# Kernel tuning notes

Hardware: AMD Instinct MI355X
Metric: run time of the kernel (lower is better)

The kernel has to match this reference:

```python
import jax, jax.numpy as jnp
import numpy as np

B, C, H, W, D = 8, 192, 128, 128, 64


def setup_inputs() -> dict:
    key = jax.random.key(0)
    ks = jax.random.split(key, 9)
    s = 0.1
    return {
        'x': jax.random.normal(ks[0], (B, C, H, W), jnp.float32),
        'Wi': jax.random.normal(ks[1], (D, C), jnp.float32) * s,   # proj_in weight
        'bi': jax.random.normal(ks[2], (D,), jnp.float32) * s,
        'W_ih': jax.random.normal(ks[3], (3 * D, D), jnp.float32) * s,  # GRUCell weight_ih (r,z,n)
        'W_hh': jax.random.normal(ks[4], (3 * D, D), jnp.float32) * s,  # GRUCell weight_hh
        'b_ih': jax.random.normal(ks[5], (3 * D,), jnp.float32) * s,
        'b_hh': jax.random.normal(ks[6], (3 * D,), jnp.float32) * s,
        'Wo': jax.random.normal(ks[7], (C, D), jnp.float32) * s,   # proj_out weight
        'bo': jax.random.normal(ks[8], (C,), jnp.float32) * s,
    }


def _gru_scan(seq, W_ih, W_hh, b_ih, b_hh):
    # seq: (N, T, D). PyTorch GRUCell gate order: r, z, n.
    N, T, Dh = seq.shape[0], seq.shape[1], W_hh.shape[1]
    x_gates = jnp.einsum('ntd,gd->ntg', seq, W_ih) + b_ih  # (N, T, 3D), precomputed
    h0 = jnp.zeros((N, Dh), seq.dtype)

    def step(h, xg):
        hg = h @ W_hh.T + b_hh
        xr, xz, xn = jnp.split(xg, 3, axis=-1)
        hr, hz, hn = jnp.split(hg, 3, axis=-1)
        r = jax.nn.sigmoid(xr + hr)
        z = jax.nn.sigmoid(xz + hz)
        n = jnp.tanh(xn + r * hn)
        h_new = (1.0 - z) * n + z * h
        return h_new, h_new

    _, hs = jax.lax.scan(step, h0, jnp.swapaxes(x_gates, 0, 1))  # (T, N, D)
    return jnp.swapaxes(hs, 0, 1)  # (N, T, D)


def _scan_direction(x, Wi, bi, W_ih, W_hh, b_ih, b_hh, Wo, bo, transpose, reverse):
    b, c, h, w = x.shape
    # arrange to (B, A, T, C): scan along T (W for row scans, H for column scans)
    xs = jnp.transpose(x, (0, 3, 2, 1)) if transpose else jnp.transpose(x, (0, 2, 3, 1))
    if reverse:
        xs = xs[:, :, ::-1, :]
    A, T = xs.shape[1], xs.shape[2]
    seq = xs.reshape(b * A, T, c) @ Wi.T + bi              # proj_in -> (N, T, D)
    hs = _gru_scan(seq, W_ih, W_hh, b_ih, b_hh)            # (N, T, D)
    out = hs @ Wo.T + bo                                   # proj_out -> (N, T, C)
    out = out.reshape(b, A, T, c)
    if reverse:
        out = out[:, :, ::-1, :]
    return jnp.transpose(out, (0, 3, 2, 1)) if transpose else jnp.transpose(out, (0, 3, 1, 2))


def reference(x, Wi, bi, W_ih, W_hh, b_ih, b_hh, Wo, bo):
    p = (Wi, bi, W_ih, W_hh, b_ih, b_hh, Wo, bo)
    right = _scan_direction(x, *p, transpose=False, reverse=False)
    down = _scan_direction(x, *p, transpose=True, reverse=False)
    left = _scan_direction(x, *p, transpose=False, reverse=True)
    up = _scan_direction(x, *p, transpose=True, reverse=True)
    return (right + down + left + up) / 4.0
```

## Files before the change

### kernel.cpp

```cpp
#include <hip/hip_runtime.h>

#define Cn   192
#define Dn   64
#define G3   192
#define HWn  16384
#define NSp  131072L
#define Tn   128

typedef unsigned short u16;
typedef __attribute__((ext_vector_type(8))) short s8v;
typedef __attribute__((ext_vector_type(4))) float f4v;

__device__ __forceinline__ float bf2f(u16 u){
  union { unsigned int i; float f; } v; v.i = ((unsigned int)u) << 16; return v.f;
}
__device__ __forceinline__ u16 f2bf(float f){
  union { float f; unsigned int u; } v; v.f = f;
  return (u16)((v.u + 0x7FFFu + ((v.u >> 16) & 1u)) >> 16);
}
__device__ __forceinline__ s8v load8_f32_as_bf16(const float* __restrict__ p){
  s8v r;
  #pragma unroll
  for (int i = 0; i < 8; i++) r[i] = (short)f2bf(p[i]);
  return r;
}
__device__ __forceinline__ float ex2f(float x){
#if __has_builtin(__builtin_amdgcn_exp2f)
  return __builtin_amdgcn_exp2f(x);
#else
  float r; asm("v_exp_f32 %0, %1" : "=v"(r) : "v"(x)); return r;
#endif
}
__device__ __forceinline__ float rcpa(float x){
#if __has_builtin(__builtin_amdgcn_rcpf)
  return __builtin_amdgcn_rcpf(x);
#else
  float r; asm("v_rcp_f32 %0, %1" : "=v"(r) : "v"(x)); return r;
#endif
}
__device__ __forceinline__ unsigned int pk2bf(float a, float b){
  unsigned int r; asm("v_cvt_pk_bf16_f32 %0, %1, %2" : "=v"(r) : "v"(a), "v"(b)); return r;
}

#define SC_RZ (-1.4426950408889634f)
#define SC_N  (-2.8853900817779268f)


__global__ __launch_bounds__(256) void k_wcomb(const float* __restrict__ Wi, const float* __restrict__ bi,
                                               const float* __restrict__ W_ih, const float* __restrict__ b_ih,
                                               const float* __restrict__ b_hh,
                                               u16* __restrict__ wcomb, float* __restrict__ bcomb){
  if (blockIdx.x < 144) {
    int idx = blockIdx.x * 256 + threadIdx.x;
    int g = idx / 192, c = idx - g * 192;
    float acc = 0.f;
    #pragma unroll 8
    for (int d = 0; d < 64; d++)
      acc += W_ih[g * 64 + d] * Wi[d * 192 + c];
    float sc = (g >= 128) ? SC_N : SC_RZ;
    wcomb[g * 192 + c] = f2bf(sc * acc);
  } else if (threadIdx.x < 192) {
    int g = threadIdx.x;
    float acc = b_ih[g];
    for (int d = 0; d < 64; d++)
      acc += W_ih[g * 64 + d] * bi[d];
    if (g < 128) acc += b_hh[g];
    float sc = (g >= 128) ? SC_N : SC_RZ;
    bcomb[g] = sc * acc;
  }
}

__global__ __launch_bounds__(256) void k_gates(const float* __restrict__ x, const u16* __restrict__ wcomb,
                                               const float* __restrict__ bcomb, u16* __restrict__ G){
  __shared__ u16 xT[64][200];
  const int tid = threadIdx.x;
  const int wave = tid >> 6, lane = tid & 63;
  const int col = lane & 15, kq = lane >> 4;
  const long s0 = (long)blockIdx.x * 64;
  const int b   = (int)(s0 >> 14);
  const int hw0 = (int)(s0 & 16383);
  const int dq  = 4 * wave + kq;

  s8v afrag[3][6];
  f4v biasv[3];
  #pragma unroll
  for (int g3 = 0; g3 < 3; g3++) {
    int g = g3 * 64 + 16 * wave + col;
    #pragma unroll
    for (int kc = 0; kc < 6; kc++)
      afrag[g3][kc] = *(const s8v*)(wcomb + g * 192 + kc * 32 + kq * 8);
    biasv[g3] = *(const f4v*)(bcomb + g3 * 64 + 16 * wave + 4 * kq);
  }

  for (int idx = tid; idx < 192 * 16; idx += 256) {
    int c  = idx >> 4;
    int s4 = (idx & 15) * 4;
    float4 v = *(const float4*)(x + (long)(b * 192 + c) * HWn + hw0 + s4);
    xT[s4 + 0][c] = f2bf(v.x); xT[s4 + 1][c] = f2bf(v.y);
    xT[s4 + 2][c] = f2bf(v.z); xT[s4 + 3][c] = f2bf(v.w);
  }
  __syncthreads();

  f4v acc[4][3];
  #pragma unroll
  for (int nt = 0; nt < 4; nt++)
    #pragma unroll
    for (int g3 = 0; g3 < 3; g3++) acc[nt][g3] = biasv[g3];

  #pragma unroll
  for (int kc = 0; kc < 6; kc++) {
    #pragma unroll
    for (int nt = 0; nt < 4; nt++) {
      s8v bx = *(const s8v*)(&xT[nt * 16 + col][kc * 32 + kq * 8]);
      #pragma unroll
      for (int g3 = 0; g3 < 3; g3++)
        acc[nt][g3] = __builtin_amdgcn_mfma_f32_16x16x32_bf16(afrag[g3][kc], bx, acc[nt][g3], 0, 0, 0);
    }
  }

  #pragma unroll
  for (int nt = 0; nt < 4; nt++) {
    long sRow = (s0 + nt * 16 + col) * 192 + dq * 12;
    #pragma unroll
    for (int g3 = 0; g3 < 3; g3++) {
      uint2 wv;
      wv.x = pk2bf(acc[nt][g3][0], acc[nt][g3][1]);
      wv.y = pk2bf(acc[nt][g3][2], acc[nt][g3][3]);
      *(uint2*)(G + sRow + g3 * 4) = wv;
    }
  }
}

__global__ __launch_bounds__(256) void k_scan(const u16* __restrict__ G, const float* __restrict__ W_hh,
                                              const float* __restrict__ b_hh, u16* __restrict__ Hall){
  __shared__ u16 ha[2][16][72];
  const int tid = threadIdx.x;
  const int w = tid >> 6, lane = tid & 63;
  const int col = lane & 15, kq = lane >> 4;
  const int dir  = blockIdx.x >> 6;
  const int sblk = blockIdx.x & 63;
  const int doff = 16 * w + 4 * kq;
  const int dq   = 4 * w + kq;

  s8v afrag[3][2];
  #pragma unroll
  for (int g3 = 0; g3 < 3; g3++) {
    float sc = (g3 == 2) ? SC_N : SC_RZ;
    const float* wr = W_hh + (g3 * 64 + 16 * w + col) * 64;
    #pragma unroll
    for (int kc = 0; kc < 2; kc++) {
      s8v f;
      #pragma unroll
      for (int i = 0; i < 8; i++) f[i] = (short)f2bf(sc * wr[kc * 32 + kq * 8 + i]);
      afrag[g3][kc] = f;
    }
  }
  f4v biasn;
  {
    const float* bb = b_hh + 128 + doff;
    biasn = (f4v){SC_N * bb[0], SC_N * bb[1], SC_N * bb[2], SC_N * bb[3]};
  }

  const int seq = sblk * 16 + col;
  const int b = seq >> 7, a = seq & 127;
  long base; int stride;
  if ((dir & 1) == 0) { base = ((long)(b * 128 + a)) * 128; stride = 1;   }
  else                { base = (long)b * 16384 + a;         stride = 128; }
  const int rev = dir >> 1;
  const long pd = rev ? -(long)stride : (long)stride;
  u16* __restrict__ Hs = Hall + (long)dir * (NSp * 64);
  const long pos0 = base + (long)(rev ? 127 : 0) * stride;
  const u16* gq = G  + pos0 * 192 + dq * 12;
  u16*       hq = Hs + pos0 * 64  + doff;

  for (int i = tid; i < 2 * 16 * 72; i += 256) ((u16*)ha)[i] = 0;

  float hold[4] = {0.f, 0.f, 0.f, 0.f};

  uint2 xr0, xz0, xn0, xr1, xz1, xn1;
  xr0 = *(const uint2*)(gq); xz0 = *(const uint2*)(gq + 4); xn0 = *(const uint2*)(gq + 8);
  gq += pd * 192;
  xr1 = *(const uint2*)(gq); xz1 = *(const uint2*)(gq + 4); xn1 = *(const uint2*)(gq + 8);
  __syncthreads();

  int p = 0;
  for (int t = 0; t < 128; t++) {
    uint2 nxr, nxz, nxn;
    if (t < 126) {
      gq += pd * 192;
      nxr = *(const uint2*)(gq); nxz = *(const uint2*)(gq + 4); nxn = *(const uint2*)(gq + 8);
    }

    s8v u0 = *(const s8v*)(&ha[p][col][kq * 8]);
    s8v u1 = *(const s8v*)(&ha[p][col][32 + kq * 8]);

    f4v acc0 = (f4v){0.f, 0.f, 0.f, 0.f};
    f4v acc1 = (f4v){0.f, 0.f, 0.f, 0.f};
    f4v acc2 = biasn;
    acc0 = __builtin_amdgcn_mfma_f32_16x16x32_bf16(afrag[0][0], u0, acc0, 0, 0, 0);
    acc1 = __builtin_amdgcn_mfma_f32_16x16x32_bf16(afrag[1][0], u0, acc1, 0, 0, 0);
    acc2 = __builtin_amdgcn_mfma_f32_16x16x32_bf16(afrag[2][0], u0, acc2, 0, 0, 0);
    acc0 = __builtin_amdgcn_mfma_f32_16x16x32_bf16(afrag[0][1], u1, acc0, 0, 0, 0);
    acc1 = __builtin_amdgcn_mfma_f32_16x16x32_bf16(afrag[1][1], u1, acc1, 0, 0, 0);
    acc2 = __builtin_amdgcn_mfma_f32_16x16x32_bf16(afrag[2][1], u1, acc2, 0, 0, 0);

    const u16* pxr = (const u16*)&xr0;
    const u16* pxz = (const u16*)&xz0;
    const u16* pxn = (const u16*)&xn0;
    float hh[4];
    #pragma unroll
    for (int r = 0; r < 4; r++) {
      float rr = rcpa(1.f + ex2f(bf2f(pxr[r]) + acc0[r]));
      float zz = rcpa(1.f + ex2f(bf2f(pxz[r]) + acc1[r]));
      float nn = 2.f * rcpa(1.f + ex2f(bf2f(pxn[r]) + rr * acc2[r])) - 1.f;
      float h  = nn + zz * (hold[r] - nn);
      hold[r] = h; hh[r] = h;
    }
    uint2 wv;
    wv.x = pk2bf(hh[0], hh[1]);
    wv.y = pk2bf(hh[2], hh[3]);
    *(uint2*)(&ha[p ^ 1][col][doff]) = wv;
    *(uint2*)(hq) = wv;
    hq += pd * 64;

    xr0 = xr1; xz0 = xz1; xn0 = xn1;
    if (t < 126) { xr1 = nxr; xz1 = nxz; xn1 = nxn; }

    asm volatile("s_waitcnt lgkmcnt(0)" ::: "memory");
    __builtin_amdgcn_s_barrier();
    __builtin_amdgcn_sched_barrier(0);
    p ^= 1;
  }
}

__global__ __launch_bounds__(256) void k_out(const u16* __restrict__ Hall, const float* __restrict__ Wo,
                                             const float* __restrict__ bo, float* __restrict__ out){
  __shared__ u16 hs4[64][72];
  const int tid = threadIdx.x;
  const int wave = tid >> 6, lane = tid & 63;
  const int col = lane & 15, kq = lane >> 4;
  const long s0 = (long)blockIdx.x * 64;
  const int b   = (int)(s0 >> 14);
  const int hw0 = (int)(s0 & 16383);

  s8v bfrag[3][2]; f4v biasf[3];
  #pragma unroll
  for (int j = 0; j < 3; j++) {
    int g = wave * 48 + j * 16 + col;
    bfrag[j][0] = load8_f32_as_bf16(Wo + g * 64 + kq * 8);
    bfrag[j][1] = load8_f32_as_bf16(Wo + g * 64 + 32 + kq * 8);
    float bb = bo[g];
    biasf[j] = (f4v){bb, bb, bb, bb};
  }

  for (int idx = tid; idx < 64 * 8; idx += 256) {
    int sl = idx >> 3;
    int d8 = (idx & 7) * 8;
    long p = (s0 + sl) * 64 + d8;
    float s[8];
    {
      uint4 v = *(const uint4*)(Hall + p);
      const u16* pv = (const u16*)&v;
      #pragma unroll
      for (int i = 0; i < 8; i++) s[i] = bf2f(pv[i]);
    }
    #pragma unroll
    for (int dd = 1; dd < 4; dd++) {
      uint4 v = *(const uint4*)(Hall + dd * (NSp * 64) + p);
      const u16* pv = (const u16*)&v;
      #pragma unroll
      for (int i = 0; i < 8; i++) s[i] += bf2f(pv[i]);
    }
    uint2 w0, w1;
    w0.x = pk2bf(0.25f * s[0], 0.25f * s[1]);
    w0.y = pk2bf(0.25f * s[2], 0.25f * s[3]);
    w1.x = pk2bf(0.25f * s[4], 0.25f * s[5]);
    w1.y = pk2bf(0.25f * s[6], 0.25f * s[7]);
    *(uint2*)(&hs4[sl][d8]) = w0;
    *(uint2*)(&hs4[sl][d8 + 4]) = w1;
  }
  __syncthreads();

  f4v acc[4][3];
  #pragma unroll
  for (int m = 0; m < 4; m++)
    #pragma unroll
    for (int j = 0; j < 3; j++) acc[m][j] = biasf[j];

  #pragma unroll
  for (int kc = 0; kc < 2; kc++) {
    #pragma unroll
    for (int m = 0; m < 4; m++) {
      s8v a = *(const s8v*)(&hs4[m * 16 + col][kc * 32 + kq * 8]);
      #pragma unroll
      for (int j = 0; j < 3; j++)
        acc[m][j] = __builtin_amdgcn_mfma_f32_16x16x32_bf16(a, bfrag[j][kc], acc[m][j], 0, 0, 0);
    }
  }

  #pragma unroll
  for (int j = 0; j < 3; j++) {
    int g = wave * 48 + j * 16 + col;
    #pragma unroll
    for (int m = 0; m < 4; m++) {
      float4 v;
      v.x = acc[m][j][0]; v.y = acc[m][j][1];
      v.z = acc[m][j][2]; v.w = acc[m][j][3];
      long addr = ((long)(b * 192 + g) << 14) + hw0 + m * 16 + kq * 4;
      *(float4*)(out + addr) = v;
    }
  }
}

extern "C" void kernel_launch(void* const* d_in, const int* in_sizes, int n_in,
                              void* d_out, int out_size, void* d_ws, size_t ws_size,
                              hipStream_t stream){
  const float* x    = (const float*)d_in[0];
  const float* Wi   = (const float*)d_in[1];
  const float* bi   = (const float*)d_in[2];
  const float* W_ih = (const float*)d_in[3];
  const float* W_hh = (const float*)d_in[4];
  const float* b_ih = (const float*)d_in[5];
  const float* b_hh = (const float*)d_in[6];
  const float* Wo   = (const float*)d_in[7];
  const float* bo   = (const float*)d_in[8];

  char* ws = (char*)d_ws;
  u16*   wcomb = (u16*)(ws);
  float* bcomb = (float*)(ws + 73728);
  u16*   G     = (u16*)(ws + 74496);
  u16*   Hall  = (u16*)(ws + 50406144);

  k_wcomb<<<145,  256, 0, stream>>>(Wi, bi, W_ih, b_ih, b_hh, wcomb, bcomb);
  k_gates<<<2048, 256, 0, stream>>>(x, wcomb, bcomb, G);
  k_scan <<<256,  256, 0, stream>>>(G, W_hh, b_hh, Hall);
  k_out  <<<2048, 256, 0, stream>>>(Hall, Wo, bo, (float*)d_out);
}
```

Before: 297.6 us.

## Swizzle gate LDS tile, unroll GRU scan by two and defer hidden-state stores

In k_gates, the x-to-LDS transpose now loads four channels at once and writes packed bf16 pairs into an XOR-swizzled LDS layout, with matching swizzled reads, to cut bank conflicts and the number of scalar stores. In the scan kernel, the time loop is unrolled by two with fixed ping-pong buffers and registers, which removes the register shuffling and the sched_barrier. Each global hidden-state store is deferred by one step so it overlaps the next step's MFMAs. The sigmoid for z and the tanh for n now share a single reciprocal computed on their product, saving one rcp per element at a small cost in numerical range and precision.

After: 329.9 us. 1.11x slower.

```diff
diff --git a/kernel.cpp b/kernel.cpp
--- a/kernel.cpp
+++ b/kernel.cpp
@@ -80,6 +80,7 @@
   const int b   = (int)(s0 >> 14);
   const int hw0 = (int)(s0 & 16383);
   const int dq  = 4 * wave + kq;
+  const int cswz = (col >> 2) << 3;
 
   s8v afrag[3][6];
   f4v biasv[3];
@@ -92,12 +93,23 @@
     biasv[g3] = *(const f4v*)(bcomb + g3 * 64 + 16 * wave + 4 * kq);
   }
 
-  for (int idx = tid; idx < 192 * 16; idx += 256) {
-    int c  = idx >> 4;
+  const float* xb = x + (long)b * 192 * HWn + hw0;
+  for (int idx = tid; idx < 768; idx += 256) {
+    int c  = (idx >> 4) * 4;
     int s4 = (idx & 15) * 4;
-    float4 v = *(const float4*)(x + (long)(b * 192 + c) * HWn + hw0 + s4);
-    xT[s4 + 0][c] = f2bf(v.x); xT[s4 + 1][c] = f2bf(v.y);
-    xT[s4 + 2][c] = f2bf(v.z); xT[s4 + 3][c] = f2bf(v.w);
+    f4v v0 = *(const f4v*)(xb + (long)(c + 0) * HWn + s4);
+    f4v v1 = *(const f4v*)(xb + (long)(c + 1) * HWn + s4);
+    f4v v2 = *(const f4v*)(xb + (long)(c + 2) * HWn + s4);
+    f4v v3 = *(const f4v*)(xb + (long)(c + 3) * HWn + s4);
+    #pragma unroll
+    for (int j = 0; j < 4; j++) {
+      int s  = s4 + j;
+      int cS = c ^ (((s >> 2) & 3) << 3);
+      uint2 wv;
+      wv.x = pk2bf(v0[j], v1[j]);
+      wv.y = pk2bf(v2[j], v3[j]);
+      *(uint2*)(&xT[s][cS]) = wv;
+    }
   }
   __syncthreads();
 
@@ -111,7 +123,7 @@
   for (int kc = 0; kc < 6; kc++) {
     #pragma unroll
     for (int nt = 0; nt < 4; nt++) {
-      s8v bx = *(const s8v*)(&xT[nt * 16 + col][kc * 32 + kq * 8]);
+      s8v bx = *(const s8v*)(&xT[nt * 16 + col][(kc * 32 + kq * 8) ^ cswz]);
       #pragma unroll
       for (int g3 = 0; g3 < 3; g3++)
         acc[nt][g3] = __builtin_amdgcn_mfma_f32_16x16x32_bf16(afrag[g3][kc], bx, acc[nt][g3], 0, 0, 0);
@@ -176,61 +188,65 @@
   for (int i = tid; i < 2 * 16 * 72; i += 256) ((u16*)ha)[i] = 0;
 
   float hold[4] = {0.f, 0.f, 0.f, 0.f};
-
-  uint2 xr0, xz0, xn0, xr1, xz1, xn1;
-  xr0 = *(const uint2*)(gq); xz0 = *(const uint2*)(gq + 4); xn0 = *(const uint2*)(gq + 8);
+  uint2 pwv = {0u, 0u};
+
+  uint2 xra, xza, xna, xrb, xzb, xnb;
+  xra = *(const uint2*)(gq); xza = *(const uint2*)(gq + 4); xna = *(const uint2*)(gq + 8);
   gq += pd * 192;
-  xr1 = *(const uint2*)(gq); xz1 = *(const uint2*)(gq + 4); xn1 = *(const uint2*)(gq + 8);
+  xrb = *(const uint2*)(gq); xzb = *(const uint2*)(gq + 4); xnb = *(const uint2*)(gq + 8);
   __syncthreads();
 
-  int p = 0;
-  for (int t = 0; t < 128; t++) {
-    uint2 nxr, nxz, nxn;
-    if (t < 126) {
-      gq += pd * 192;
-      nxr = *(const uint2*)(gq); nxz = *(const uint2*)(gq + 4); nxn = *(const uint2*)(gq + 8);
-    }
-
-    s8v u0 = *(const s8v*)(&ha[p][col][kq * 8]);
-    s8v u1 = *(const s8v*)(&ha[p][col][32 + kq * 8]);
-
-    f4v acc0 = (f4v){0.f, 0.f, 0.f, 0.f};
-    f4v acc1 = (f4v){0.f, 0.f, 0.f, 0.f};
-    f4v acc2 = biasn;
-    acc0 = __builtin_amdgcn_mfma_f32_16x16x32_bf16(afrag[0][0], u0, acc0, 0, 0, 0);
-    acc1 = __builtin_amdgcn_mfma_f32_16x16x32_bf16(afrag[1][0], u0, acc1, 0, 0, 0);
-    acc2 = __builtin_amdgcn_mfma_f32_16x16x32_bf16(afrag[2][0], u0, acc2, 0, 0, 0);
-    acc0 = __builtin_amdgcn_mfma_f32_16x16x32_bf16(afrag[0][1], u1, acc0, 0, 0, 0);
-    acc1 = __builtin_amdgcn_mfma_f32_16x16x32_bf16(afrag[1][1], u1, acc1, 0, 0, 0);
-    acc2 = __builtin_amdgcn_mfma_f32_16x16x32_bf16(afrag[2][1], u1, acc2, 0, 0, 0);
-
-    const u16* pxr = (const u16*)&xr0;
-    const u16* pxz = (const u16*)&xz0;
-    const u16* pxn = (const u16*)&xn0;
-    float hh[4];
-    #pragma unroll
-    for (int r = 0; r < 4; r++) {
-      float rr = rcpa(1.f + ex2f(bf2f(pxr[r]) + acc0[r]));
-      float zz = rcpa(1.f + ex2f(bf2f(pxz[r]) + acc1[r]));
-      float nn = 2.f * rcpa(1.f + ex2f(bf2f(pxn[r]) + rr * acc2[r])) - 1.f;
-      float h  = nn + zz * (hold[r] - nn);
-      hold[r] = h; hh[r] = h;
-    }
-    uint2 wv;
-    wv.x = pk2bf(hh[0], hh[1]);
-    wv.y = pk2bf(hh[2], hh[3]);
-    *(uint2*)(&ha[p ^ 1][col][doff]) = wv;
-    *(uint2*)(hq) = wv;
-    hq += pd * 64;
-
-    xr0 = xr1; xz0 = xz1; xn0 = xn1;
-    if (t < 126) { xr1 = nxr; xz1 = nxz; xn1 = nxn; }
-
-    asm volatile("s_waitcnt lgkmcnt(0)" ::: "memory");
-    __builtin_amdgcn_s_barrier();
-    __builtin_amdgcn_sched_barrier(0);
-    p ^= 1;
-  }
+  #define SCAN_STEP(P, XR, XZ, XN, T)                                              \
+  do {                                                                             \
+    s8v u0 = *(const s8v*)(&ha[(P)][col][kq * 8]);                                 \
+    s8v u1 = *(const s8v*)(&ha[(P)][col][32 + kq * 8]);                            \
+    if ((T) > 0) { *(uint2*)hq = pwv; hq += pd * 64; }        \
+    f4v acc0 = (f4v){0.f, 0.f, 0.f, 0.f};                                          \
+    f4v acc1 = (f4v){0.f, 0.f, 0.f, 0.f};                                          \
+    f4v acc2 = biasn;                                                              \
+    acc0 = __builtin_amdgcn_mfma_f32_16x16x32_bf16(afrag[0][0], u0, acc0, 0, 0, 0);\
+    acc1 = __builtin_amdgcn_mfma_f32_16x16x32_bf16(afrag[1][0], u0, acc1, 0, 0, 0);\
+    acc2 = __builtin_amdgcn_mfma_f32_16x16x32_bf16(afrag[2][0], u0, acc2, 0, 0, 0);\
+    acc0 = __builtin_amdgcn_mfma_f32_16x16x32_bf16(afrag[0][1], u1, acc0, 0, 0, 0);\
+    acc1 = __builtin_amdgcn_mfma_f32_16x16x32_bf16(afrag[1][1], u1, acc1, 0, 0, 0);\
+    acc2 = __builtin_amdgcn_mfma_f32_16x16x32_bf16(afrag[2][1], u1, acc2, 0, 0, 0);\
+    const u16* pxr = (const u16*)&XR;                                              \
+    const u16* pxz = (const u16*)&XZ;                                              \
+    const u16* pxn = (const u16*)&XN;                                              \
+    float hh[4];                                                                   \
+    _Pragma("unroll")                                                              \
+    for (int r = 0; r < 4; r++) {                                                  \
+      float erv = ex2f(bf2f(pxr[r]) + acc0[r]);                                    \
+      float rrv = rcpa(1.f + erv);                                                 \
+      float ezv = ex2f(bf2f(pxz[r]) + acc1[r]);                                    \
+      float dzv = 1.f + ezv;                                                       \
+      float env = ex2f(bf2f(pxn[r]) + rrv * acc2[r]);                              \
+      float dnv = 1.f + env;                                                       \
+      float qv  = rcpa(dzv * dnv);                      \
+      float zzv = qv * dnv;                                       \
+      float nnv = __builtin_fmaf(dzv + dzv, qv, -1.f);          \
+      float h   = __builtin_fmaf(zzv, hold[r] - nnv, nnv);                         \
+      hold[r] = h; hh[r] = h;                                                      \
+    }                                                                              \
+    uint2 wv;                                                                      \
+    wv.x = pk2bf(hh[0], hh[1]);                                                    \
+    wv.y = pk2bf(hh[2], hh[3]);                                                    \
+    *(uint2*)(&ha[(P) ^ 1][col][doff]) = wv;                                       \
+    pwv = wv;                                                                      \
+    if ((T) < 126) {                        \
+      gq += pd * 192;                                                              \
+      XR = *(const uint2*)(gq); XZ = *(const uint2*)(gq + 4); XN = *(const uint2*)(gq + 8); \
+    }                                                                              \
+    asm volatile("s_waitcnt lgkmcnt(0)" ::: "memory");                             \
+    __builtin_amdgcn_s_barrier();                                                  \
+  } while (0)
+
+  for (int t = 0; t < 128; t += 2) {
+    SCAN_STEP(0, xra, xza, xna, t);
+    SCAN_STEP(1, xrb, xzb, xnb, t + 1);
+  }
+  *(uint2*)hq = pwv;
+  #undef SCAN_STEP
 }
 
 __global__ __launch_bounds__(256) void k_out(const u16* __restrict__ Hall, const float* __restrict__ Wo,
```

## Swizzle gate-GEMM LDS layout, pack 4-channel stores, share GRU reciprocal

Applied to the files above, without the earlier changes.

In the input-gate kernel, each thread now loads four channels per spatial position and writes packed bf16 pairs as 64-bit stores into an XOR-swizzled LDS tile, and the MFMA operand reads apply the same swizzle. This is meant to cut LDS bank conflicts and the number of scalar 16-bit LDS stores. In the recurrent step, the z and n sigmoids now share one reciprocal of the product of their denominators, replacing three reciprocals with two plus a few multiplies and FMAs. The shared reciprocal adds a little rounding difference and could overflow if the exponentials are very large.

After: 289.8 us. -2.6%, faster.

```diff
diff --git a/kernel.cpp b/kernel.cpp
--- a/kernel.cpp
+++ b/kernel.cpp
@@ -80,6 +80,7 @@
   const int b   = (int)(s0 >> 14);
   const int hw0 = (int)(s0 & 16383);
   const int dq  = 4 * wave + kq;
+  const int cswz = (col >> 2) << 3;
 
   s8v afrag[3][6];
   f4v biasv[3];
@@ -92,12 +93,23 @@
     biasv[g3] = *(const f4v*)(bcomb + g3 * 64 + 16 * wave + 4 * kq);
   }
 
-  for (int idx = tid; idx < 192 * 16; idx += 256) {
-    int c  = idx >> 4;
+  const float* xb = x + (long)b * 192 * HWn + hw0;
+  for (int idx = tid; idx < 768; idx += 256) {
+    int c  = (idx >> 4) * 4;
     int s4 = (idx & 15) * 4;
-    float4 v = *(const float4*)(x + (long)(b * 192 + c) * HWn + hw0 + s4);
-    xT[s4 + 0][c] = f2bf(v.x); xT[s4 + 1][c] = f2bf(v.y);
-    xT[s4 + 2][c] = f2bf(v.z); xT[s4 + 3][c] = f2bf(v.w);
+    f4v v0 = *(const f4v*)(xb + (long)(c + 0) * HWn + s4);
+    f4v v1 = *(const f4v*)(xb + (long)(c + 1) * HWn + s4);
+    f4v v2 = *(const f4v*)(xb + (long)(c + 2) * HWn + s4);
+    f4v v3 = *(const f4v*)(xb + (long)(c + 3) * HWn + s4);
+    #pragma unroll
+    for (int j = 0; j < 4; j++) {
+      int s  = s4 + j;
+      int cS = c ^ (((s >> 2) & 3) << 3);
+      uint2 wv;
+      wv.x = pk2bf(v0[j], v1[j]);
+      wv.y = pk2bf(v2[j], v3[j]);
+      *(uint2*)(&xT[s][cS]) = wv;
+    }
   }
   __syncthreads();
 
@@ -111,7 +123,7 @@
   for (int kc = 0; kc < 6; kc++) {
     #pragma unroll
     for (int nt = 0; nt < 4; nt++) {
-      s8v bx = *(const s8v*)(&xT[nt * 16 + col][kc * 32 + kq * 8]);
+      s8v bx = *(const s8v*)(&xT[nt * 16 + col][(kc * 32 + kq * 8) ^ cswz]);
       #pragma unroll
       for (int g3 = 0; g3 < 3; g3++)
         acc[nt][g3] = __builtin_amdgcn_mfma_f32_16x16x32_bf16(afrag[g3][kc], bx, acc[nt][g3], 0, 0, 0);
@@ -210,10 +222,16 @@
     float hh[4];
     #pragma unroll
     for (int r = 0; r < 4; r++) {
-      float rr = rcpa(1.f + ex2f(bf2f(pxr[r]) + acc0[r]));
-      float zz = rcpa(1.f + ex2f(bf2f(pxz[r]) + acc1[r]));
-      float nn = 2.f * rcpa(1.f + ex2f(bf2f(pxn[r]) + rr * acc2[r])) - 1.f;
-      float h  = nn + zz * (hold[r] - nn);
+      float erv = ex2f(bf2f(pxr[r]) + acc0[r]);
+      float rrv = rcpa(1.f + erv);
+      float ezv = ex2f(bf2f(pxz[r]) + acc1[r]);
+      float dzv = 1.f + ezv;
+      float env = ex2f(bf2f(pxn[r]) + rrv * acc2[r]);
+      float dnv = 1.f + env;
+      float qv  = rcpa(dzv * dnv);
+      float zzv = qv * dnv;
+      float nnv = __builtin_fmaf(dzv + dzv, qv, -1.f);
+      float h   = __builtin_fmaf(zzv, hold[r] - nnv, nnv);
       hold[r] = h; hh[r] = h;
     }
     uint2 wv;
```
